# Kernel tuning notes

Hardware: AMD Instinct MI355X
Metric: run time of the kernel (lower is better)

## Reference

```python
import jax, jax.numpy as jnp
import numpy as np

N = 100000      # nodes
E = 1280000     # edges
D_IN = 64       # in_channels
D_OUT = 64      # out_channels
D_EDGE = 16     # edge_dim
NEG_SLOPE = 0.01  # torch F.leaky_relu default


def setup_inputs() -> dict:
    key = jax.random.key(0)
    ks = jax.random.split(key, 8)
    x = jax.random.normal(ks[0], (N, D_IN), dtype=jnp.float32)
    edge_attr = jax.random.normal(ks[1], (E, D_EDGE), dtype=jnp.float32)
    src = jax.random.randint(ks[2], (E,), 0, N, dtype=jnp.int32)
    dst = jax.random.randint(ks[3], (E,), 0, N, dtype=jnp.int32)
    # parameters (xavier-like scale)
    W1 = jax.random.normal(ks[4], (D_OUT, D_IN + D_EDGE), dtype=jnp.float32) * (2.0 / (D_OUT + D_IN + D_EDGE)) ** 0.5
    W2 = jax.random.normal(ks[5], (D_OUT, D_IN), dtype=jnp.float32) * (2.0 / (D_OUT + D_IN)) ** 0.5
    attn = jax.random.normal(ks[6], (D_OUT + D_IN,), dtype=jnp.float32) * (2.0 / (1 + D_OUT + D_IN)) ** 0.5
    bias = jnp.zeros((D_OUT,), dtype=jnp.float32)
    return {"x": x, "edge_attr": edge_attr, "src": src, "dst": dst,
            "W1": W1, "W2": W2, "attn": attn, "bias": bias}


def reference(x, edge_attr, src, dst, W1, W2, attn, bias):
    # node transform: lin2
    x_t = x @ W2.T                                    # [N, D_OUT]
    # per-edge gathers
    x_l = x[src]                                      # [E, D_IN]
    x_r = x[dst]                                      # [E, D_IN]
    # lin1 on [x_l || edge_attr]
    f_srt = jnp.concatenate([x_l, edge_attr], axis=-1) @ W1.T   # [E, D_OUT]
    e = jax.nn.leaky_relu(jnp.concatenate([f_srt, x_r], axis=-1), NEG_SLOPE)  # [E, D_OUT+D_IN]
    logits = e @ attn                                 # [E]
    # edge_softmax over destination-node segments
    seg_max = jax.ops.segment_max(logits, dst, num_segments=N)
    seg_max = jnp.where(jnp.isfinite(seg_max), seg_max, 0.0)
    expd = jnp.exp(logits - seg_max[dst])             # [E]
    denom = jax.ops.segment_sum(expd, dst, num_segments=N)
    alpha = expd / denom[dst]                         # [E]  (dropout p=0 -> identity)
    # scatter-sum aggregation: sum_e alpha_e * x_t[src_e] into dst
    msgs = x_t[src] * alpha[:, None]                  # [E, D_OUT]
    h = jax.ops.segment_sum(msgs, dst, num_segments=N)
    return h + bias
```

## Files before the change

### kernel.cpp

```cpp
#include <hip/hip_runtime.h>

#define D 64
#define D_EDGE 16
#define NEG 0.01f

typedef unsigned int  uint32;
typedef unsigned short ushort16;

__device__ __forceinline__ float leaky(float v) { return fmaxf(v, NEG * v); }

__device__ __forceinline__ ushort16 f2bf(float f) {
    uint32 b = __float_as_uint(f);
    uint32 r = b + 0x7fffu + ((b >> 16) & 1u);
    return (ushort16)(r >> 16);
}
__device__ __forceinline__ float bf2f(ushort16 u) {
    return __uint_as_float(((uint32)u) << 16);
}
__device__ __forceinline__ float bf_lo(uint32 w) { return __uint_as_float(w << 16); }
__device__ __forceinline__ float bf_hi(uint32 w) { return __uint_as_float(w & 0xffff0000u); }

__global__ __launch_bounds__(256) void node_kernel(
    const float* __restrict__ x, const float* __restrict__ W1,
    const float* __restrict__ W2,
    ushort16* __restrict__ Abf, ushort16* __restrict__ xtb, int N_)
{
    __shared__ float w2s[64 * 64];
    __shared__ float w1s[64 * 64];
    for (int i = threadIdx.x; i < 64 * 64; i += 256) {
        w2s[i] = W2[i];
        int k = i >> 6, j = i & 63;
        w1s[i] = W1[k * 80 + j];
    }
    __syncthreads();

    const int lane = threadIdx.x & 63;
    const int q    = threadIdx.x >> 6;
    const int n    = blockIdx.x * 64 + lane;
    if (n >= N_) return;

    const float4* x4 = (const float4*)(x + (size_t)n * D);
    float4 xr[16];
#pragma unroll
    for (int i = 0; i < 16; i++) xr[i] = x4[i];

    const float4* w2s4 = (const float4*)w2s;
    const float4* w1s4 = (const float4*)w1s;

    uint32* Au = (uint32*)Abf;
    uint32* Xu = (uint32*)xtb;

    float a_prev = 0.f, b_prev = 0.f;
#pragma unroll
    for (int kk = 0; kk < 16; kk++) {
        const int k = q * 16 + kk;
        float a = 0.f, b = 0.f;
#pragma unroll
        for (int j = 0; j < 16; j++) {
            float4 w = w2s4[k * 16 + j];
            a += xr[j].x * w.x + xr[j].y * w.y + xr[j].z * w.z + xr[j].w * w.w;
            float4 u = w1s4[k * 16 + j];
            b += xr[j].x * u.x + xr[j].y * u.y + xr[j].z * u.z + xr[j].w * u.w;
        }
        if (kk & 1) {
            Xu[(size_t)n * 32 + (k >> 1)] = (uint32)f2bf(a_prev) | ((uint32)f2bf(a) << 16);
            Au[(size_t)n * 32 + (k >> 1)] = (uint32)f2bf(b_prev) | ((uint32)f2bf(b) << 16);
        } else {
            a_prev = a; b_prev = b;
        }
    }
}

__global__ __launch_bounds__(256) void hist_kernel(
    const int* __restrict__ dst, int* __restrict__ cnt, int E_)
{
    int i = blockIdx.x * 256 + threadIdx.x;
    if (i < E_) atomicAdd(cnt + dst[i], 1);
}

__global__ __launch_bounds__(256) void scan1(
    const int* __restrict__ cnt, int* __restrict__ part, int N_)
{
    __shared__ int sm[256];
    const int b = blockIdx.x, t = threadIdx.x;
    const int i0 = b * 1024 + t * 4;
    int s = 0;
    if (i0     < N_) s += cnt[i0];
    if (i0 + 1 < N_) s += cnt[i0 + 1];
    if (i0 + 2 < N_) s += cnt[i0 + 2];
    if (i0 + 3 < N_) s += cnt[i0 + 3];
    sm[t] = s; __syncthreads();
    for (int off = 128; off > 0; off >>= 1) {
        if (t < off) sm[t] += sm[t + off];
        __syncthreads();
    }
    if (t == 0) part[b] = sm[0];
}

__global__ __launch_bounds__(256) void scan2(int* __restrict__ part, int nb)
{
    __shared__ int sm[256];
    const int t = threadIdx.x;
    int v = (t < nb) ? part[t] : 0;
    sm[t] = v; __syncthreads();
    for (int off = 1; off < 256; off <<= 1) {
        int a = (t >= off) ? sm[t - off] : 0;
        __syncthreads();
        sm[t] += a;
        __syncthreads();
    }
    if (t < nb) part[t] = sm[t] - v;
}

__global__ __launch_bounds__(256) void scan3(
    const int* __restrict__ cnt, const int* __restrict__ part,
    int* __restrict__ rowst, int N_)
{
    __shared__ int sm[256];
    const int b = blockIdx.x, t = threadIdx.x;
    const int i0 = b * 1024 + t * 4;
    int c0 = 0, c1 = 0, c2 = 0, c3 = 0;
    if (i0     < N_) c0 = cnt[i0];
    if (i0 + 1 < N_) c1 = cnt[i0 + 1];
    if (i0 + 2 < N_) c2 = cnt[i0 + 2];
    if (i0 + 3 < N_) c3 = cnt[i0 + 3];
    const int s = c0 + c1 + c2 + c3;
    sm[t] = s; __syncthreads();
    for (int off = 1; off < 256; off <<= 1) {
        int a = (t >= off) ? sm[t - off] : 0;
        __syncthreads();
        sm[t] += a;
        __syncthreads();
    }
    const int base = part[b] + (sm[t] - s);
    if (i0     < N_) rowst[i0]     = base;
    if (i0 + 1 < N_) rowst[i0 + 1] = base + c0;
    if (i0 + 2 < N_) rowst[i0 + 2] = base + c0 + c1;
    if (i0 + 3 < N_) rowst[i0 + 3] = base + c0 + c1 + c2;
}

__global__ __launch_bounds__(256) void edge_kernel(
    const float* __restrict__ edge_attr, const int* __restrict__ src,
    const int* __restrict__ dst, const float* __restrict__ W1,
    const float* __restrict__ attn, const ushort16* __restrict__ Abf,
    int* __restrict__ rowpos, int2* __restrict__ SP, int E_)
{
    const int e = blockIdx.x * 256 + threadIdx.x;
    if (e >= E_) return;

    const int s = src[e];
    const int d = dst[e];

    uint32 Ad[32];
    {
        const uint4* Ap = (const uint4*)(Abf + (size_t)s * D);
#pragma unroll
        for (int i = 0; i < 8; i++) *(uint4*)(Ad + 4 * i) = Ap[i];
    }
    float Ef[16];
    {
        const float4* Ep = (const float4*)(edge_attr + (size_t)e * D_EDGE);
#pragma unroll
        for (int i = 0; i < 4; i++) *(float4*)(Ef + 4 * i) = Ep[i];
    }

    float v = 0.f;
#pragma unroll
    for (int j = 0; j < 32; ++j) {
        const float4* w0 = (const float4*)(W1 + (2 * j) * 80 + 64);
        const float4* w1 = (const float4*)(W1 + (2 * j + 1) * 80 + 64);
        float4 p0 = w0[0], p1 = w0[1], p2 = w0[2], p3 = w0[3];
        float4 q0 = w1[0], q1 = w1[1], q2 = w1[2], q3 = w1[3];

        float g0 = bf_lo(Ad[j]);
        float g1 = bf_hi(Ad[j]);

        g0 = fmaf(Ef[ 0], p0.x, g0); g1 = fmaf(Ef[ 0], q0.x, g1);
        g0 = fmaf(Ef[ 1], p0.y, g0); g1 = fmaf(Ef[ 1], q0.y, g1);
        g0 = fmaf(Ef[ 2], p0.z, g0); g1 = fmaf(Ef[ 2], q0.z, g1);
        g0 = fmaf(Ef[ 3], p0.w, g0); g1 = fmaf(Ef[ 3], q0.w, g1);
        g0 = fmaf(Ef[ 4], p1.x, g0); g1 = fmaf(Ef[ 4], q1.x, g1);
        g0 = fmaf(Ef[ 5], p1.y, g0); g1 = fmaf(Ef[ 5], q1.y, g1);
        g0 = fmaf(Ef[ 6], p1.z, g0); g1 = fmaf(Ef[ 6], q1.z, g1);
        g0 = fmaf(Ef[ 7], p1.w, g0); g1 = fmaf(Ef[ 7], q1.w, g1);
        g0 = fmaf(Ef[ 8], p2.x, g0); g1 = fmaf(Ef[ 8], q2.x, g1);
        g0 = fmaf(Ef[ 9], p2.y, g0); g1 = fmaf(Ef[ 9], q2.y, g1);
        g0 = fmaf(Ef[10], p2.z, g0); g1 = fmaf(Ef[10], q2.z, g1);
        g0 = fmaf(Ef[11], p2.w, g0); g1 = fmaf(Ef[11], q2.w, g1);
        g0 = fmaf(Ef[12], p3.x, g0); g1 = fmaf(Ef[12], q3.x, g1);
        g0 = fmaf(Ef[13], p3.y, g0); g1 = fmaf(Ef[13], q3.y, g1);
        g0 = fmaf(Ef[14], p3.z, g0); g1 = fmaf(Ef[14], q3.z, g1);
        g0 = fmaf(Ef[15], p3.w, g0); g1 = fmaf(Ef[15], q3.w, g1);

        v = fmaf(leaky(g0), attn[2 * j],     v);
        v = fmaf(leaky(g1), attn[2 * j + 1], v);
    }

    const float p = __expf(v);
    const int pos = atomicAdd(rowpos + d, 1);
    SP[pos] = make_int2(s, __float_as_int(p));
}

__global__ __launch_bounds__(256) void agg_kernel(
    const ushort16* __restrict__ xtb, const int2* __restrict__ SP,
    const int* __restrict__ rowend, const float* __restrict__ bias,
    float* __restrict__ out, int N_)
{
    const int n    = blockIdx.x * 4 + (threadIdx.x >> 6);
    const int lane = threadIdx.x & 63;
    if (n >= N_) return;

    const int end   = rowend[n];
    const int start = n ? rowend[n - 1] : 0;

    float acc = 0.f, den = 0.f;
    int i = start;
    for (; i + 3 < end; i += 4) {
        int2 a = SP[i], b = SP[i + 1], c = SP[i + 2], d = SP[i + 3];
        float pa = __int_as_float(a.y), pb = __int_as_float(b.y);
        float pc = __int_as_float(c.y), pd = __int_as_float(d.y);
        float ma = bf2f(xtb[(size_t)a.x * D + lane]);
        float mb = bf2f(xtb[(size_t)b.x * D + lane]);
        float mc = bf2f(xtb[(size_t)c.x * D + lane]);
        float md = bf2f(xtb[(size_t)d.x * D + lane]);
        acc = fmaf(pa, ma, fmaf(pb, mb, fmaf(pc, mc, fmaf(pd, md, acc))));
        den += (pa + pb) + (pc + pd);
    }
    for (; i < end; i++) {
        int2 a = SP[i];
        float pa = __int_as_float(a.y);
        acc = fmaf(pa, bf2f(xtb[(size_t)a.x * D + lane]), acc);
        den += pa;
    }

    float sc = den > 0.f ? 1.f / den : 0.f;
    out[(size_t)n * D + lane] = fmaf(acc, sc, bias[lane]);
}

extern "C" void kernel_launch(void* const* d_in, const int* in_sizes, int n_in,
                              void* d_out, int out_size, void* d_ws, size_t ws_size,
                              hipStream_t stream)
{
    const float* x         = (const float*)d_in[0];
    const float* edge_attr = (const float*)d_in[1];
    const int*   src       = (const int*)d_in[2];
    const int*   dst       = (const int*)d_in[3];
    const float* W1        = (const float*)d_in[4];
    const float* W2        = (const float*)d_in[5];
    const float* attn      = (const float*)d_in[6];
    const float* bias      = (const float*)d_in[7];
    float* out = (float*)d_out;

    const int N_ = in_sizes[0] / D;
    const int E_ = in_sizes[2];

    char* w = (char*)d_ws;
    ushort16* Abf  = (ushort16*)w;  w += (size_t)N_ * D * sizeof(ushort16);
    ushort16* xtb  = (ushort16*)w;  w += (size_t)N_ * D * sizeof(ushort16);
    int2*     SP   = (int2*)w;      w += (size_t)E_ * sizeof(int2);
    int*      rowst= (int*)w;       w += (size_t)N_ * sizeof(int);
    int*      cnt  = (int*)w;       w += (size_t)N_ * sizeof(int);
    int*      part = (int*)w;

    hipMemsetAsync(cnt, 0, (size_t)N_ * sizeof(int), stream);

    const int NB1 = (N_ + 1023) / 1024;

    hist_kernel<<<(E_ + 255) / 256, 256, 0, stream>>>(dst, cnt, E_);
    scan1<<<NB1, 256, 0, stream>>>(cnt, part, N_);
    scan2<<<1, 256, 0, stream>>>(part, NB1);
    scan3<<<NB1, 256, 0, stream>>>(cnt, part, rowst, N_);

    node_kernel<<<(N_ + 63) / 64, 256, 0, stream>>>(x, W1, W2, Abf, xtb, N_);

    edge_kernel<<<(E_ + 255) / 256, 256, 0, stream>>>(edge_attr, src, dst, W1,
                                                      attn, Abf, rowst, SP, E_);

    agg_kernel<<<(N_ + 3) / 4, 256, 0, stream>>>(xtb, SP, rowst, bias, out, N_);
}
```

Measured before the change: 409.8 us.

## Stage x in LDS, process two edges per thread, and split agg rows across half-waves

The node kernel now stages a tile of x rows in LDS and reads the weights straight from global memory with wave-uniform indices, so they can be served by scalar loads, instead of copying W1/W2 into LDS. The edge kernel handles two edges per thread, which reuses each weight load across both and raises memory-level parallelism, at the cost of more registers. The aggregation kernel has each half-wave process alternate edges with packed bf16 pair loads and combines them with a cross-half shuffle, doubling the gathers in flight per row. Each change targets a different kernel's latency or load overhead.

```diff
diff --git a/kernel.cpp b/kernel.cpp
--- a/kernel.cpp
+++ b/kernel.cpp
@@ -20,32 +20,44 @@
 __device__ __forceinline__ float bf_lo(uint32 w) { return __uint_as_float(w << 16); }
 __device__ __forceinline__ float bf_hi(uint32 w) { return __uint_as_float(w & 0xffff0000u); }
 
+__device__ __forceinline__ float dot16(const float* Ef, float4 p0, float4 p1,
+                                       float4 p2, float4 p3, float g) {
+    g = fmaf(Ef[ 0], p0.x, g); g = fmaf(Ef[ 1], p0.y, g);
+    g = fmaf(Ef[ 2], p0.z, g); g = fmaf(Ef[ 3], p0.w, g);
+    g = fmaf(Ef[ 4], p1.x, g); g = fmaf(Ef[ 5], p1.y, g);
+    g = fmaf(Ef[ 6], p1.z, g); g = fmaf(Ef[ 7], p1.w, g);
+    g = fmaf(Ef[ 8], p2.x, g); g = fmaf(Ef[ 9], p2.y, g);
+    g = fmaf(Ef[10], p2.z, g); g = fmaf(Ef[11], p2.w, g);
+    g = fmaf(Ef[12], p3.x, g); g = fmaf(Ef[13], p3.y, g);
+    g = fmaf(Ef[14], p3.z, g); g = fmaf(Ef[15], p3.w, g);
+    return g;
+}
+
 __global__ __launch_bounds__(256) void node_kernel(
     const float* __restrict__ x, const float* __restrict__ W1,
     const float* __restrict__ W2,
     ushort16* __restrict__ Abf, ushort16* __restrict__ xtb, int N_)
 {
-    __shared__ float w2s[64 * 64];
-    __shared__ float w1s[64 * 64];
-    for (int i = threadIdx.x; i < 64 * 64; i += 256) {
-        w2s[i] = W2[i];
-        int k = i >> 6, j = i & 63;
-        w1s[i] = W1[k * 80 + j];
+    __shared__ float xs[64][68];
+    const int tid = threadIdx.x;
+    const int b0  = blockIdx.x * 64;
+
+    for (int idx = tid; idx < 64 * 16; idx += 256) {
+        const int rr = idx >> 4, cc = idx & 15;
+        float4 v = make_float4(0.f, 0.f, 0.f, 0.f);
+        if (b0 + rr < N_) v = ((const float4*)(x + (size_t)(b0 + rr) * D))[cc];
+        *(float4*)&xs[rr][cc * 4] = v;
     }
     __syncthreads();
 
-    const int lane = threadIdx.x & 63;
-    const int q    = threadIdx.x >> 6;
-    const int n    = blockIdx.x * 64 + lane;
+    const int lane = tid & 63;
+    const int q    = __builtin_amdgcn_readfirstlane(tid >> 6);
+    const int n    = b0 + lane;
     if (n >= N_) return;
 
-    const float4* x4 = (const float4*)(x + (size_t)n * D);
     float4 xr[16];
 #pragma unroll
-    for (int i = 0; i < 16; i++) xr[i] = x4[i];
-
-    const float4* w2s4 = (const float4*)w2s;
-    const float4* w1s4 = (const float4*)w1s;
+    for (int i = 0; i < 16; i++) xr[i] = *(const float4*)&xs[lane][4 * i];
 
     uint32* Au = (uint32*)Abf;
     uint32* Xu = (uint32*)xtb;
@@ -54,12 +66,14 @@
 #pragma unroll
     for (int kk = 0; kk < 16; kk++) {
         const int k = q * 16 + kk;
+        const float4* w2r = (const float4*)(W2 + (size_t)k * 64);
+        const float4* w1r = (const float4*)(W1 + (size_t)k * 80);
         float a = 0.f, b = 0.f;
 #pragma unroll
         for (int j = 0; j < 16; j++) {
-            float4 w = w2s4[k * 16 + j];
+            float4 w = w2r[j];
             a += xr[j].x * w.x + xr[j].y * w.y + xr[j].z * w.z + xr[j].w * w.w;
-            float4 u = w1s4[k * 16 + j];
+            float4 u = w1r[j];
             b += xr[j].x * u.x + xr[j].y * u.y + xr[j].z * u.z + xr[j].w * u.w;
         }
         if (kk & 1) {
@@ -145,60 +159,75 @@
     const float* __restrict__ attn, const ushort16* __restrict__ Abf,
     int* __restrict__ rowpos, int2* __restrict__ SP, int E_)
 {
-    const int e = blockIdx.x * 256 + threadIdx.x;
-    if (e >= E_) return;
-
-    const int s = src[e];
-    const int d = dst[e];
-
-    uint32 Ad[32];
-    {
-        const uint4* Ap = (const uint4*)(Abf + (size_t)s * D);
-#pragma unroll
-        for (int i = 0; i < 8; i++) *(uint4*)(Ad + 4 * i) = Ap[i];
-    }
-    float Ef[16];
-    {
-        const float4* Ep = (const float4*)(edge_attr + (size_t)e * D_EDGE);
-#pragma unroll
-        for (int i = 0; i < 4; i++) *(float4*)(Ef + 4 * i) = Ep[i];
-    }
-
-    float v = 0.f;
+    const int e0 = blockIdx.x * 512 + threadIdx.x;
+    const int e1 = e0 + 256;
+    const bool ok0 = e0 < E_;
+    const bool ok1 = e1 < E_;
+
+    int s0 = 0, d0 = 0, s1 = 0, d1 = 0;
+    if (ok0) { s0 = src[e0]; d0 = dst[e0]; }
+    if (ok1) { s1 = src[e1]; d1 = dst[e1]; }
+
+    uint32 Ad0[32], Ad1[32];
+    float  Ef0[16], Ef1[16];
+
+    if (ok0) {
+        const uint4* Ap = (const uint4*)(Abf + (size_t)s0 * D);
+#pragma unroll
+        for (int i = 0; i < 8; i++) *(uint4*)(Ad0 + 4 * i) = Ap[i];
+        const float4* Ep = (const float4*)(edge_attr + (size_t)e0 * D_EDGE);
+#pragma unroll
+        for (int i = 0; i < 4; i++) *(float4*)(Ef0 + 4 * i) = Ep[i];
+    } else {
+#pragma unroll
+        for (int i = 0; i < 32; i++) Ad0[i] = 0;
+#pragma unroll
+        for (int i = 0; i < 16; i++) Ef0[i] = 0.f;
+    }
+    if (ok1) {
+        const uint4* Ap = (const uint4*)(Abf + (size_t)s1 * D);
+#pragma unroll
+        for (int i = 0; i < 8; i++) *(uint4*)(Ad1 + 4 * i) = Ap[i];
+        const float4* Ep = (const float4*)(edge_attr + (size_t)e1 * D_EDGE);
+#pragma unroll
+        for (int i = 0; i < 4; i++) *(float4*)(Ef1 + 4 * i) = Ep[i];
+    } else {
+#pragma unroll
+        for (int i = 0; i < 32; i++) Ad1[i] = 0;
+#pragma unroll
+        for (int i = 0; i < 16; i++) Ef1[i] = 0.f;
+    }
+
+    float v0 = 0.f, v1 = 0.f;
 #pragma unroll
     for (int j = 0; j < 32; ++j) {
-        const float4* w0 = (const float4*)(W1 + (2 * j) * 80 + 64);
-        const float4* w1 = (const float4*)(W1 + (2 * j + 1) * 80 + 64);
-        float4 p0 = w0[0], p1 = w0[1], p2 = w0[2], p3 = w0[3];
-        float4 q0 = w1[0], q1 = w1[1], q2 = w1[2], q3 = w1[3];
-
-        float g0 = bf_lo(Ad[j]);
-        float g1 = bf_hi(Ad[j]);
-
-        g0 = fmaf(Ef[ 0], p0.x, g0); g1 = fmaf(Ef[ 0], q0.x, g1);
-        g0 = fmaf(Ef[ 1], p0.y, g0); g1 = fmaf(Ef[ 1], q0.y, g1);
-        g0 = fmaf(Ef[ 2], p0.z, g0); g1 = fmaf(Ef[ 2], q0.z, g1);
-        g0 = fmaf(Ef[ 3], p0.w, g0); g1 = fmaf(Ef[ 3], q0.w, g1);
-        g0 = fmaf(Ef[ 4], p1.x, g0); g1 = fmaf(Ef[ 4], q1.x, g1);
-        g0 = fmaf(Ef[ 5], p1.y, g0); g1 = fmaf(Ef[ 5], q1.y, g1);
-        g0 = fmaf(Ef[ 6], p1.z, g0); g1 = fmaf(Ef[ 6], q1.z, g1);
-        g0 = fmaf(Ef[ 7], p1.w, g0); g1 = fmaf(Ef[ 7], q1.w, g1);
-        g0 = fmaf(Ef[ 8], p2.x, g0); g1 = fmaf(Ef[ 8], q2.x, g1);
-        g0 = fmaf(Ef[ 9], p2.y, g0); g1 = fmaf(Ef[ 9], q2.y, g1);
-        g0 = fmaf(Ef[10], p2.z, g0); g1 = fmaf(Ef[10], q2.z, g1);
-        g0 = fmaf(Ef[11], p2.w, g0); g1 = fmaf(Ef[11], q2.w, g1);
-        g0 = fmaf(Ef[12], p3.x, g0); g1 = fmaf(Ef[12], q3.x, g1);
-        g0 = fmaf(Ef[13], p3.y, g0); g1 = fmaf(Ef[13], q3.y, g1);
-        g0 = fmaf(Ef[14], p3.z, g0); g1 = fmaf(Ef[14], q3.z, g1);
-        g0 = fmaf(Ef[15], p3.w, g0); g1 = fmaf(Ef[15], q3.w, g1);
-
-        v = fmaf(leaky(g0), attn[2 * j],     v);
-        v = fmaf(leaky(g1), attn[2 * j + 1], v);
-    }
-
-    const float p = __expf(v);
-    const int pos = atomicAdd(rowpos + d, 1);
-    SP[pos] = make_int2(s, __float_as_int(p));
+        const float4* wA = (const float4*)(W1 + (size_t)(2 * j) * 80 + 64);
+        const float4* wB = (const float4*)(W1 + (size_t)(2 * j + 1) * 80 + 64);
+        float4 p0 = wA[0], p1 = wA[1], p2 = wA[2], p3 = wA[3];
+        float4 q0 = wB[0], q1 = wB[1], q2 = wB[2], q3 = wB[3];
+        const float ak0 = attn[2 * j], ak1 = attn[2 * j + 1];
+
+        float g00 = dot16(Ef0, p0, p1, p2, p3, bf_lo(Ad0[j]));
+        float g01 = dot16(Ef0, q0, q1, q2, q3, bf_hi(Ad0[j]));
+        float g10 = dot16(Ef1, p0, p1, p2, p3, bf_lo(Ad1[j]));
+        float g11 = dot16(Ef1, q0, q1, q2, q3, bf_hi(Ad1[j]));
+
+        v0 = fmaf(leaky(g00), ak0, v0);
+        v0 = fmaf(leaky(g01), ak1, v0);
+        v1 = fmaf(leaky(g10), ak0, v1);
+        v1 = fmaf(leaky(g11), ak1, v1);
+    }
+
+    if (ok0) {
+        const float p = __expf(v0);
+        const int pos = atomicAdd(rowpos + d0, 1);
+        SP[pos] = make_int2(s0, __float_as_int(p));
+    }
+    if (ok1) {
+        const float p = __expf(v1);
+        const int pos = atomicAdd(rowpos + d1, 1);
+        SP[pos] = make_int2(s1, __float_as_int(p));
+    }
 }
 
 __global__ __launch_bounds__(256) void agg_kernel(
@@ -209,32 +238,54 @@
     const int n    = blockIdx.x * 4 + (threadIdx.x >> 6);
     const int lane = threadIdx.x & 63;
     if (n >= N_) return;
+    const int half = lane >> 5;
+    const int c    = lane & 31;
 
     const int end   = rowend[n];
     const int start = n ? rowend[n - 1] : 0;
-
-    float acc = 0.f, den = 0.f;
+    const uint32* X = (const uint32*)xtb;
+
+    float accx = 0.f, accy = 0.f, den = 0.f;
     int i = start;
-    for (; i + 3 < end; i += 4) {
-        int2 a = SP[i], b = SP[i + 1], c = SP[i + 2], d = SP[i + 3];
-        float pa = __int_as_float(a.y), pb = __int_as_float(b.y);
-        float pc = __int_as_float(c.y), pd = __int_as_float(d.y);
-        float ma = bf2f(xtb[(size_t)a.x * D + lane]);
-        float mb = bf2f(xtb[(size_t)b.x * D + lane]);
-        float mc = bf2f(xtb[(size_t)c.x * D + lane]);
-        float md = bf2f(xtb[(size_t)d.x * D + lane]);
-        acc = fmaf(pa, ma, fmaf(pb, mb, fmaf(pc, mc, fmaf(pd, md, acc))));
-        den += (pa + pb) + (pc + pd);
+    for (; i + 7 < end; i += 8) {
+        int2 A0 = SP[i+0], A1 = SP[i+1], A2 = SP[i+2], A3 = SP[i+3];
+        int2 A4 = SP[i+4], A5 = SP[i+5], A6 = SP[i+6], A7 = SP[i+7];
+        int   r0 = half ? A1.x : A0.x;  float p0 = __int_as_float(half ? A1.y : A0.y);
+        int   r1 = half ? A3.x : A2.x;  float p1 = __int_as_float(half ? A3.y : A2.y);
+        int   r2 = half ? A5.x : A4.x;  float p2 = __int_as_float(half ? A5.y : A4.y);
+        int   r3 = half ? A7.x : A6.x;  float p3 = __int_as_float(half ? A7.y : A6.y);
+        uint32 u0 = X[(size_t)r0 * 32 + c];
+        uint32 u1 = X[(size_t)r1 * 32 + c];
+        uint32 u2 = X[(size_t)r2 * 32 + c];
+        uint32 u3 = X[(size_t)r3 * 32 + c];
+        accx = fmaf(p0, bf_lo(u0), accx); accy = fmaf(p0, bf_hi(u0), accy);
+        accx = fmaf(p1, bf_lo(u1), accx); accy = fmaf(p1, bf_hi(u1), accy);
+        accx = fmaf(p2, bf_lo(u2), accx); accy = fmaf(p2, bf_hi(u2), accy);
+        accx = fmaf(p3, bf_lo(u3), accx); accy = fmaf(p3, bf_hi(u3), accy);
+        den += (p0 + p1) + (p2 + p3);
     }
     for (; i < end; i++) {
         int2 a = SP[i];
-        float pa = __int_as_float(a.y);
-        acc = fmaf(pa, bf2f(xtb[(size_t)a.x * D + lane]), acc);
-        den += pa;
-    }
-
-    float sc = den > 0.f ? 1.f / den : 0.f;
-    out[(size_t)n * D + lane] = fmaf(acc, sc, bias[lane]);
+        if (half == 0) {
+            float p = __int_as_float(a.y);
+            uint32 u = X[(size_t)a.x * 32 + c];
+            accx = fmaf(p, bf_lo(u), accx);
+            accy = fmaf(p, bf_hi(u), accy);
+            den += p;
+        }
+    }
+    accx += __shfl_xor(accx, 32, 64);
+    accy += __shfl_xor(accy, 32, 64);
+    den  += __shfl_xor(den,  32, 64);
+
+    if (half == 0) {
+        const float sc = den > 0.f ? 1.f / den : 0.f;
+        const float2 bb = *(const float2*)(bias + 2 * c);
+        float2 o;
+        o.x = fmaf(accx, sc, bb.x);
+        o.y = fmaf(accy, sc, bb.y);
+        *(float2*)(out + (size_t)n * D + 2 * c) = o;
+    }
 }
 
 extern "C" void kernel_launch(void* const* d_in, const int* in_sizes, int n_in,
@@ -273,7 +324,7 @@
 
     node_kernel<<<(N_ + 63) / 64, 256, 0, stream>>>(x, W1, W2, Abf, xtb, N_);
 
-    edge_kernel<<<(E_ + 255) / 256, 256, 0, stream>>>(edge_attr, src, dst, W1,
+    edge_kernel<<<(E_ + 511) / 512, 256, 0, stream>>>(edge_attr, src, dst, W1,
                                                       attn, Abf, rowst, SP, E_);
 
     agg_kernel<<<(N_ + 3) / 4, 256, 0, stream>>>(xtb, SP, rowst, bias, out, N_);
```

After: 526.9 us. 1.29x slower.
